# Kernel tuning notes

Hardware: AMD Instinct MI355X
Metric: run time of the kernel (lower is better)

## Reference

```python
import jax, jax.numpy as jnp
import numpy as np

NB_CLASSES = 10
EPS = 1e-8  # torch cosine_similarity eps


def gcn_conv(x, W, b, src, dst, n):
    h = x @ W
    deg = jax.ops.segment_sum(jnp.ones_like(src, dtype=h.dtype), dst, num_segments=n) + 1.0
    dinv = deg ** -0.5
    coef = (dinv[src] * dinv[dst])[:, None]
    agg = jax.ops.segment_sum(h[src] * coef, dst, num_segments=n)
    return agg + h * (1.0 / deg)[:, None] + b


def condition_net(e, w_in, b_in, w_hid, b_hid, w_out, b_out):
    # ConditionNet with num_layers=2: input_fc -> elu -> hidden_fc[0] -> elu -> output_fc
    h = jax.nn.elu(e @ w_in + b_in)
    h = jax.nn.elu(h @ w_hid + b_hid)
    return h @ w_out + b_out


def setup_inputs() -> dict:
    key = jax.random.key(0)
    N, E, D, H, T, M = 20000, 320000, 256, 256, 3, 2048
    ks = jax.random.split(key, 24)
    s = 1.0 / np.sqrt(D)
    inp = {
        "x": jax.random.normal(ks[0], (N, D), dtype=jnp.float32),
        "src": jax.random.randint(ks[1], (E,), 0, N, dtype=jnp.int32),
        "dst": jax.random.randint(ks[2], (E,), 0, N, dtype=jnp.int32),
        "idx": jax.random.randint(ks[3], (M,), 0, N, dtype=jnp.int32),
        "labels": jax.random.randint(ks[4], (M,), 0, NB_CLASSES, dtype=jnp.int32),
        "train": 1,
        # 3 GCNConv layers (all D->D, residual structure forces equal widths)
        "gcn_W1": jax.random.normal(ks[5], (D, D), dtype=jnp.float32) * s,
        "gcn_b1": jnp.zeros((D,), dtype=jnp.float32),
        "gcn_W2": jax.random.normal(ks[6], (D, D), dtype=jnp.float32) * s,
        "gcn_b2": jnp.zeros((D,), dtype=jnp.float32),
        "gcn_W3": jax.random.normal(ks[7], (D, D), dtype=jnp.float32) * s,
        "gcn_b3": jnp.zeros((D,), dtype=jnp.float32),
        # T=3 ConditionNets, params stacked on leading axis
        "cn_w_in": jax.random.normal(ks[8], (T, D, H), dtype=jnp.float32) * s,
        "cn_b_in": jnp.zeros((T, H), dtype=jnp.float32),
        "cn_w_hid": jax.random.normal(ks[9], (T, H, H), dtype=jnp.float32) * s,
        "cn_b_hid": jnp.zeros((T, H), dtype=jnp.float32),
        "cn_w_out": jax.random.normal(ks[10], (T, H, D), dtype=jnp.float32) * s,
        "cn_b_out": jnp.zeros((T, D), dtype=jnp.float32),
        # Embed_prompt
        "p_list": jax.random.normal(ks[11], (5, D), dtype=jnp.float32) * s,
        "a_W": jax.random.normal(ks[12], (D, 5), dtype=jnp.float32) * s,
        "a_b": jnp.zeros((5,), dtype=jnp.float32),
        # gcn_weight2 (trainable); weight1 and weight3 are frozen zeros, closed over
        "gcn_weight2": jnp.float32(1.0),
    }
    return inp


def reference(x, src, dst, idx, labels, train,
              gcn_W1, gcn_b1, gcn_W2, gcn_b2, gcn_W3, gcn_b3,
              cn_w_in, cn_b_in, cn_w_hid, cn_b_hid, cn_w_out, cn_b_out,
              p_list, a_W, a_b, gcn_weight2):
    n = x.shape[0]
    origin_x = x
    w1 = jnp.float32(0.0)  # gcn_weight1 (frozen)
    w3 = jnp.float32(0.0)  # gcn_weight3 (frozen)
    T = cn_w_in.shape[0]
    for t in range(T):  # think layers (small static count)
        e1 = gcn_conv(x, gcn_W1, gcn_b1, src, dst, n)
        e2 = gcn_conv(e1, gcn_W2, gcn_b2, src, dst, n) + e1
        e3 = gcn_conv(e2, gcn_W3, gcn_b3, src, dst, n) + e2
        embed = w1 * e1 + gcn_weight2 * e2 + w3 * e3
        prompt = condition_net(embed, cn_w_in[t], cn_b_in[t], cn_w_hid[t], cn_b_hid[t],
                               cn_w_out[t], cn_b_out[t])
        x = prompt * origin_x
    # full gcn(x, edge_index): 3 convs with ELU activation (standard GCN forward)
    h = jax.nn.elu(gcn_conv(x, gcn_W1, gcn_b1, src, dst, n))
    h = jax.nn.elu(gcn_conv(h, gcn_W2, gcn_b2, src, dst, n))
    h = jax.nn.elu(gcn_conv(h, gcn_W3, gcn_b3, src, dst, n))
    # Embed_prompt: attention over 5 learned prompt vectors
    weight = jax.nn.softmax(h @ a_W + a_b, axis=1)  # [N, 5]
    embed = h + weight @ p_list
    rawret = embed[idx]  # [M, D]
    # train==1: class prototypes via scatter-mean over labels
    sums = jax.ops.segment_sum(rawret, labels, num_segments=NB_CLASSES)
    counts = jax.ops.segment_sum(jnp.ones_like(labels, dtype=rawret.dtype), labels,
                                 num_segments=NB_CLASSES)
    ave = sums / jnp.maximum(counts, 1.0)[:, None]  # [C, D]
    # fused cosine similarity: normalize both, one matmul (replaces M*C scalar loop)
    rn = rawret / jnp.maximum(jnp.linalg.norm(rawret, axis=1, keepdims=True), EPS)
    an = ave / jnp.maximum(jnp.linalg.norm(ave, axis=1, keepdims=True), EPS)
    ret = jax.nn.softmax(rn @ an.T, axis=1)  # [M, C]
    return ret
```

## Files before the change

### kernel.cpp

```cpp
#include <hip/hip_runtime.h>
#include <hip/hip_bf16.h>
#include <math.h>

#define NN 20000
#define DD 256
#define EE 320000
#define MM 2048
#define CC 10
#define TT 3

typedef __attribute__((ext_vector_type(8))) short s8v;
typedef __attribute__((ext_vector_type(4))) float f4v;

__device__ unsigned short g_xb[NN * DD];
__device__ unsigned short g_xo[NN * DD];
__device__ unsigned short g_hb[NN * DD];
__device__ unsigned short g_e1b[NN * DD];
__device__ unsigned short g_e2b[NN * DD];
__device__ int   g_cnt[NN];
__device__ int   g_cursor[NN];
__device__ int   g_rowstart[NN + 1];
__device__ float g_dinv[NN];
__device__ float g_invdeg[NN];
__device__ int   g_part[128];
__device__ int2  g_edge[EE];
__device__ float g_sums[CC * DD];
__device__ float g_cntf[CC];
__device__ unsigned short g_wT1[12 * DD * DD];
__device__ unsigned short g_wT2[12 * DD * DD];

__device__ __forceinline__ float wave_sum(float v) {
#pragma unroll
  for (int off = 32; off > 0; off >>= 1) v += __shfl_xor(v, off);
  return v;
}

__device__ __forceinline__ float eluf(float x) {
  return x > 0.f ? x : expm1f(x);
}

__device__ __forceinline__ float2 bfpair(unsigned int d) {
  union { unsigned int i; float f; } a, b;
  a.i = d << 16;
  b.i = d & 0xffff0000u;
  return make_float2(a.f, b.f);
}

__device__ __forceinline__ unsigned int packbf(float x, float y) {
  union { __hip_bfloat162 v; unsigned int u; } c;
  c.v = __float22bfloat162_rn(make_float2(x, y));
  return c.u;
}

__device__ __forceinline__ void gl_lds16(const unsigned short* g, unsigned short* l) {
  __builtin_amdgcn_global_load_lds(
      (const __attribute__((address_space(1))) unsigned int*)g,
      (__attribute__((address_space(3))) unsigned int*)l, 16, 0, 0);
}

struct WPtrs { const float* p[12]; };

__global__ __launch_bounds__(256) void init_k(const float* __restrict__ x,
                                              unsigned short* __restrict__ xb,
                                              WPtrs wp) {
  __shared__ float t[64][65];
  int b = blockIdx.x;
  int tid = threadIdx.x;
  if (b < 2500) {
    int i = b * 256 + tid;
    const float4* x4 = (const float4*)x;
    float4 a = x4[i * 2], bb = x4[i * 2 + 1];
    uint4 o;
    o.x = packbf(a.x, a.y);
    o.y = packbf(a.z, a.w);
    o.z = packbf(bb.x, bb.y);
    o.w = packbf(bb.z, bb.w);
    ((uint4*)xb)[i] = o;
  } else if (b < 2692) {
    int bb = b - 2500;
    int widx = bb >> 4;
    int rem = bb & 15;
    int kt0 = (rem >> 2) * 64, nt0 = (rem & 3) * 64;
    const float* W = wp.p[widx];
    int ln = tid & 63, lk = tid >> 6;
    for (int kk = lk; kk < 64; kk += 4)
      t[kk][ln] = W[(size_t)(kt0 + kk) * DD + nt0 + ln];
    __syncthreads();
    for (int nn = lk; nn < 64; nn += 4) {
      float v = t[ln][nn];
      __hip_bfloat16 hb = __float2bfloat16(v);
      float hf = __bfloat162float(hb);
      __hip_bfloat16 lb = __float2bfloat16(v - hf);
      union { __hip_bfloat16 b; unsigned short s; } ch, cl;
      ch.b = hb; cl.b = lb;
      size_t o = (size_t)widx * DD * DD + (size_t)(nt0 + nn) * DD + kt0 + ln;
      g_wT1[o] = ch.s;
      g_wT2[o] = cl.s;
    }
  } else {
    int i = (b - 2692) * 256 + tid;
    if (i < NN) { g_cnt[i] = 0; g_cursor[i] = 0; }
    if (i < CC * DD) g_sums[i] = 0.f;
    if (i < CC) g_cntf[i] = 0.f;
  }
}

__global__ void hist_k(const int* __restrict__ dst) {
  int e = blockIdx.x * blockDim.x + threadIdx.x;
  if (e < EE) atomicAdd(&g_cnt[dst[e]], 1);
}

__global__ __launch_bounds__(256) void scanA_k() {
  __shared__ int s[256];
  int t = threadIdx.x;
  int i = blockIdx.x * 256 + t;
  int v = (i < NN) ? g_cnt[i] : 0;
  s[t] = v;
  __syncthreads();
#pragma unroll
  for (int off = 128; off > 0; off >>= 1) {
    if (t < off) s[t] += s[t + off];
    __syncthreads();
  }
  if (t == 0) g_part[blockIdx.x] = s[0];
}

__global__ __launch_bounds__(256) void scanC_k() {
  __shared__ int ps[128];
  __shared__ int s[256];
  int t = threadIdx.x;
  if (t < 128) ps[t] = (t < 79) ? g_part[t] : 0;
  __syncthreads();
#pragma unroll
  for (int off = 1; off < 128; off <<= 1) {
    int v = (t >= off && t < 128) ? ps[t - off] : 0;
    __syncthreads();
    if (t < 128) ps[t] += v;
    __syncthreads();
  }
  int base = (blockIdx.x == 0) ? 0 : ps[blockIdx.x - 1];
  int i = blockIdx.x * 256 + t;
  int v = (i < NN) ? g_cnt[i] : 0;
  s[t] = v;
  __syncthreads();
#pragma unroll
  for (int off = 1; off < 256; off <<= 1) {
    int x2 = (t >= off) ? s[t - off] : 0;
    __syncthreads();
    s[t] += x2;
    __syncthreads();
  }
  if (i < NN) {
    g_rowstart[i] = base + s[t] - v;
    float dg = (float)(v + 1);
    g_invdeg[i] = 1.0f / dg;
    g_dinv[i] = 1.0f / sqrtf(dg);
  }
  if (blockIdx.x == 78 && t == 0) g_rowstart[NN] = EE;
}

__global__ void fill_k(const int* __restrict__ src, const int* __restrict__ dst) {
  int e = blockIdx.x * blockDim.x + threadIdx.x;
  if (e < EE) {
    int d = dst[e];
    int p = atomicAdd(&g_cursor[d], 1);
    int j = g_rowstart[d] + p;
    int si = src[e];
    float coef = g_dinv[si] * g_dinv[d];
    g_edge[j] = make_int2(si * 512, __float_as_int(coef));
  }
}

template <int SPLIT>
union GemmSM {
  unsigned short st[2][(1024 + 512 * SPLIT) * 8];
  float ct[64][68];
};

template <int EPI, int SPLIT>
__global__ __launch_bounds__(256) void gemm_k(const unsigned short* __restrict__ A,
                                              const unsigned short* __restrict__ B1,
                                              const unsigned short* __restrict__ B2,
                                              unsigned short* __restrict__ C,
                                              const float* __restrict__ bias,
                                              const float* __restrict__ alphap,
                                              const unsigned short* __restrict__ mul) {
  __shared__ GemmSM<SPLIT> sm;
  constexpr int CB = 1024 + 512 * SPLIT;
  int b = blockIdx.x;
  int xcd = b & 7, off = b >> 3;
  int logical = (xcd < 4) ? xcd * 157 + off : 628 + (xcd - 4) * 156 + off;
  int mblk = logical >> 2, nblk = logical & 3;
  int row0 = mblk * 64, col0 = nblk * 64;

  int tid = threadIdx.x;
  int wv = tid >> 6, lane = tid & 63;
  int wm = wv >> 1, wn = wv & 1;
  int lr = lane & 15, lk = lane >> 4;

  f4v acc[2][2];
#pragma unroll
  for (int i = 0; i < 2; ++i)
#pragma unroll
    for (int j = 0; j < 2; ++j) acc[i][j] = (f4v){0.f, 0.f, 0.f, 0.f};

  auto stage = [&](int buf, int kt) {
    unsigned short* base = sm.st[buf];
#pragma unroll
    for (int i = 0; i < CB / 256; ++i) {
      int cb = (wv * (CB / 256) + i) * 64;
      int c = cb + lane;
      unsigned short* ldst = base + (size_t)cb * 8;
      if (c < 512) {
        int row = c >> 3, pos = c & 7;
        int kc = pos ^ (row & 7);
        int gr = row0 + row;
        gr = gr < NN ? gr : NN - 1;
        gl_lds16(A + (size_t)gr * DD + kt + kc * 8, ldst);
      } else if (c < 1024) {
        int c2 = c - 512;
        int col = c2 >> 3, pos = c2 & 7;
        int kc = pos ^ (col & 7);
        gl_lds16(B1 + (size_t)(col0 + col) * DD + kt + kc * 8, ldst);
      } else {
        int c2 = c - 1024;
        int col = c2 >> 3, pos = c2 & 7;
        int kc = pos ^ (col & 7);
        gl_lds16(B2 + (size_t)(col0 + col) * DD + kt + kc * 8, ldst);
      }
    }
  };

  stage(0, 0);
  __syncthreads();

  int buf = 0;
#pragma unroll
  for (int t = 0; t < 4; ++t) {
    if (t < 3) stage(buf ^ 1, (t + 1) * 64);
    const unsigned short* base = sm.st[buf];
#pragma unroll
    for (int ksub = 0; ksub < 2; ++ksub) {
      int kc = ksub * 4 + lk;
      s8v a[2], b1v[2], b2v[2];
#pragma unroll
      for (int mi = 0; mi < 2; ++mi) {
        int row = wm * 32 + mi * 16 + lr;
        a[mi] = *(const s8v*)(base + (row * 8 + (kc ^ (row & 7))) * 8);
      }
#pragma unroll
      for (int nj = 0; nj < 2; ++nj) {
        int col = wn * 32 + nj * 16 + lr;
        int ch = col * 8 + (kc ^ (col & 7));
        b1v[nj] = *(const s8v*)(base + (512 + ch) * 8);
        if (SPLIT) b2v[nj] = *(const s8v*)(base + (1024 + ch) * 8);
      }
#pragma unroll
      for (int mi = 0; mi < 2; ++mi)
#pragma unroll
        for (int nj = 0; nj < 2; ++nj) {
          acc[mi][nj] = __builtin_amdgcn_mfma_f32_16x16x32_bf16(a[mi], b1v[nj], acc[mi][nj], 0, 0, 0);
          if (SPLIT)
            acc[mi][nj] = __builtin_amdgcn_mfma_f32_16x16x32_bf16(a[mi], b2v[nj], acc[mi][nj], 0, 0, 0);
        }
    }
    __syncthreads();
    buf ^= 1;
  }

#pragma unroll
  for (int mi = 0; mi < 2; ++mi)
#pragma unroll
    for (int nj = 0; nj < 2; ++nj)
#pragma unroll
      for (int r = 0; r < 4; ++r)
        sm.ct[wm * 32 + mi * 16 + lk * 4 + r][wn * 32 + nj * 16 + lr] = acc[mi][nj][r];
  __syncthreads();

  float alpha = 1.f;
  if (EPI == 1) alpha = alphap ? *alphap : 1.f;
#pragma unroll
  for (int p = 0; p < 2; ++p) {
    int row = p * 32 + (tid >> 3);
    int c0 = (tid & 7) * 8;
    int gr = row0 + row;
    int gc = col0 + c0;
    if (gr < NN) {
      float v[8];
      float4 va = *(float4*)&sm.ct[row][c0];
      float4 vb = *(float4*)&sm.ct[row][c0 + 4];
      v[0] = va.x; v[1] = va.y; v[2] = va.z; v[3] = va.w;
      v[4] = vb.x; v[5] = vb.y; v[6] = vb.z; v[7] = vb.w;
      if (EPI == 1) {
        float4 bv0 = *(const float4*)(bias + gc);
        float4 bv1 = *(const float4*)(bias + gc + 4);
        float bb[8] = {bv0.x, bv0.y, bv0.z, bv0.w, bv1.x, bv1.y, bv1.z, bv1.w};
#pragma unroll
        for (int i = 0; i < 8; ++i) v[i] = eluf(fmaf(alpha, v[i], bb[i]));
      } else if (EPI == 2) {
        float4 bv0 = *(const float4*)(bias + gc);
        float4 bv1 = *(const float4*)(bias + gc + 4);
        float bb[8] = {bv0.x, bv0.y, bv0.z, bv0.w, bv1.x, bv1.y, bv1.z, bv1.w};
        uint4 mu = *(const uint4*)(mul + (size_t)gr * DD + gc);
        float2 m0 = bfpair(mu.x), m1 = bfpair(mu.y), m2 = bfpair(mu.z), m3 = bfpair(mu.w);
        float mm[8] = {m0.x, m0.y, m1.x, m1.y, m2.x, m2.y, m3.x, m3.y};
#pragma unroll
        for (int i = 0; i < 8; ++i) v[i] = (v[i] + bb[i]) * mm[i];
      }
      uint4 o;
      o.x = packbf(v[0], v[1]);
      o.y = packbf(v[2], v[3]);
      o.z = packbf(v[4], v[5]);
      o.w = packbf(v[6], v[7]);
      *(uint4*)(C + (size_t)gr * DD + gc) = o;
    }
  }
}

template <int RES>
__device__ __forceinline__ void agg_row8(int row, int sl, int hf,
                                         const unsigned short* __restrict__ h,
                                         const float* __restrict__ bias,
                                         const unsigned short* __restrict__ res,
                                         float* o) {
  const char* hb = (const char*)h;
  int lo = sl * 16;
  float acc[8];
#pragma unroll
  for (int k = 0; k < 8; ++k) acc[k] = 0.f;
  int s = g_rowstart[row], e = g_rowstart[row + 1];
  int j = s;
  for (; j + 12 <= e; j += 12) {
    int2 E[6];
    uint4 V[6];
#pragma unroll
    for (int u = 0; u < 6; ++u) E[u] = g_edge[j + 2 * u + hf];
#pragma unroll
    for (int u = 0; u < 6; ++u) V[u] = *(const uint4*)(hb + (size_t)E[u].x + lo);
#pragma unroll
    for (int u = 0; u < 6; ++u) {
      float c = __int_as_float(E[u].y);
      float2 p0 = bfpair(V[u].x), p1 = bfpair(V[u].y);
      float2 p2 = bfpair(V[u].z), p3 = bfpair(V[u].w);
      acc[0] = fmaf(c, p0.x, acc[0]); acc[1] = fmaf(c, p0.y, acc[1]);
      acc[2] = fmaf(c, p1.x, acc[2]); acc[3] = fmaf(c, p1.y, acc[3]);
      acc[4] = fmaf(c, p2.x, acc[4]); acc[5] = fmaf(c, p2.y, acc[5]);
      acc[6] = fmaf(c, p3.x, acc[6]); acc[7] = fmaf(c, p3.y, acc[7]);
    }
  }
  for (; j < e; j += 2) {
    int jj = j + hf;
    int jc = jj < e ? jj : e - 1;
    int2 E0 = g_edge[jc];
    uint4 V0 = *(const uint4*)(hb + (size_t)E0.x + lo);
    float c = (jj < e) ? __int_as_float(E0.y) : 0.f;
    float2 p0 = bfpair(V0.x), p1 = bfpair(V0.y);
    float2 p2 = bfpair(V0.z), p3 = bfpair(V0.w);
    acc[0] = fmaf(c, p0.x, acc[0]); acc[1] = fmaf(c, p0.y, acc[1]);
    acc[2] = fmaf(c, p1.x, acc[2]); acc[3] = fmaf(c, p1.y, acc[3]);
    acc[4] = fmaf(c, p2.x, acc[4]); acc[5] = fmaf(c, p2.y, acc[5]);
    acc[6] = fmaf(c, p3.x, acc[6]); acc[7] = fmaf(c, p3.y, acc[7]);
  }
#pragma unroll
  for (int k = 0; k < 8; ++k) acc[k] += __shfl_xor(acc[k], 32);
  float idg = g_invdeg[row];
  uint4 hv = *(const uint4*)(hb + (size_t)row * 512 + lo);
  float2 h0 = bfpair(hv.x), h1 = bfpair(hv.y), h2 = bfpair(hv.z), h3 = bfpair(hv.w);
  float hw[8] = {h0.x, h0.y, h1.x, h1.y, h2.x, h2.y, h3.x, h3.y};
  float4 b0 = *(const float4*)(bias + sl * 8);
  float4 b1 = *(const float4*)(bias + sl * 8 + 4);
  float bb[8] = {b0.x, b0.y, b0.z, b0.w, b1.x, b1.y, b1.z, b1.w};
#pragma unroll
  for (int k = 0; k < 8; ++k) o[k] = acc[k] + hw[k] * idg + bb[k];
  if (RES) {
    uint4 rv = *(const uint4*)((const char*)res + (size_t)row * 512 + lo);
    float2 r0 = bfpair(rv.x), r1 = bfpair(rv.y), r2 = bfpair(rv.z), r3 = bfpair(rv.w);
    float rw[8] = {r0.x, r0.y, r1.x, r1.y, r2.x, r2.y, r3.x, r3.y};
#pragma unroll
    for (int k = 0; k < 8; ++k) o[k] += rw[k];
  }
}

template <int ELU, int RES>
__global__ __launch_bounds__(256) void agg_k(const unsigned short* __restrict__ h,
                                             const float* __restrict__ bias,
                                             const unsigned short* __restrict__ res,
                                             unsigned short* __restrict__ out) {
  int row = (blockIdx.x * 256 + threadIdx.x) >> 6;
  int lane = threadIdx.x & 63;
  int sl = lane & 31, hf = lane >> 5;
  float o[8];
  agg_row8<RES>(row, sl, hf, h, bias, res, o);
  if (ELU) {
#pragma unroll
    for (int k = 0; k < 8; ++k) o[k] = eluf(o[k]);
  }
  if (hf == 0) {
    uint4 pk;
    pk.x = packbf(o[0], o[1]);
    pk.y = packbf(o[2], o[3]);
    pk.z = packbf(o[4], o[5]);
    pk.w = packbf(o[6], o[7]);
    *(uint4*)((char*)out + (size_t)row * 512 + sl * 16) = pk;
  }
}

__device__ __forceinline__ float4 attn_apply(float4 r, int lane,
                                             const float* __restrict__ aW,
                                             const float* __restrict__ ab,
                                             const float* __restrict__ plist) {
  int d = lane * 4;
  float lg[5];
#pragma unroll
  for (int k = 0; k < 5; ++k) {
    float p = r.x * aW[(d + 0) * 5 + k] + r.y * aW[(d + 1) * 5 + k] +
              r.z * aW[(d + 2) * 5 + k] + r.w * aW[(d + 3) * 5 + k];
    lg[k] = wave_sum(p) + ab[k];
  }
  float mx = lg[0];
#pragma unroll
  for (int k = 1; k < 5; ++k) mx = fmaxf(mx, lg[k]);
  float w[5], sum = 0.f;
#pragma unroll
  for (int k = 0; k < 5; ++k) { w[k] = expf(lg[k] - mx); sum += w[k]; }
  float inv = 1.f / sum;
#pragma unroll
  for (int k = 0; k < 5; ++k) {
    float wk = w[k] * inv;
    float4 pv = *(const float4*)(plist + k * DD + d);
    r.x = fmaf(wk, pv.x, r.x);
    r.y = fmaf(wk, pv.y, r.y);
    r.z = fmaf(wk, pv.z, r.z);
    r.w = fmaf(wk, pv.w, r.w);
  }
  return r;
}

__global__ __launch_bounds__(256) void proto_k(const unsigned short* __restrict__ h,
                                               const int* __restrict__ idxp,
                                               const int* __restrict__ labels,
                                               const float* __restrict__ aW,
                                               const float* __restrict__ ab,
                                               const float* __restrict__ plist) {
  __shared__ float sums[CC][DD];
  __shared__ float cnts[CC];
  int t = threadIdx.x;
#pragma unroll
  for (int c = 0; c < CC; ++c) sums[c][t] = 0.f;
  if (t < CC) cnts[t] = 0.f;
  __syncthreads();
  int wv = t >> 6, lane = t & 63;
  int m0 = blockIdx.x * 64 + wv * 16;
  int d = lane * 4;
  for (int rr = 0; rr < 16; ++rr) {
    int m = m0 + rr;
    int row = idxp[m];
    int lab = labels[m];
    uint2 rv = *(const uint2*)((const char*)h + (size_t)row * 512 + lane * 8);
    float2 a0 = bfpair(rv.x), a1 = bfpair(rv.y);
    float4 r = attn_apply(make_float4(a0.x, a0.y, a1.x, a1.y), lane, aW, ab, plist);
    atomicAdd(&sums[lab][d + 0], r.x);
    atomicAdd(&sums[lab][d + 1], r.y);
    atomicAdd(&sums[lab][d + 2], r.z);
    atomicAdd(&sums[lab][d + 3], r.w);
    if (lane == 0) atomicAdd(&cnts[lab], 1.f);
  }
  __syncthreads();
#pragma unroll
  for (int c = 0; c < CC; ++c) atomicAdd(&g_sums[c * DD + t], sums[c][t]);
  if (t < CC) atomicAdd(&g_cntf[t], cnts[t]);
}

__global__ __launch_bounds__(256) void cos_k(const unsigned short* __restrict__ h,
                                             const int* __restrict__ idxp,
                                             const float* __restrict__ aW,
                                             const float* __restrict__ ab,
                                             const float* __restrict__ plist,
                                             float* __restrict__ out) {
  __shared__ float an[CC][DD];
  __shared__ float red[4];
  int t = threadIdx.x;
  int lane = t & 63, wv = t >> 6;
  for (int c = 0; c < CC; ++c) {
    float v = g_sums[c * DD + t] / fmaxf(g_cntf[c], 1.0f);
    float sq = wave_sum(v * v);
    if (lane == 0) red[wv] = sq;
    __syncthreads();
    float tot = red[0] + red[1] + red[2] + red[3];
    float nrm = fmaxf(sqrtf(tot), 1e-8f);
    an[c][t] = v / nrm;
    __syncthreads();
  }
  int wid = (blockIdx.x * 256 + t) >> 6;
  if (wid >= MM) return;
  int row = idxp[wid];
  uint2 rv = *(const uint2*)((const char*)h + (size_t)row * 512 + lane * 8);
  float2 r0 = bfpair(rv.x), r1 = bfpair(rv.y);
  float4 r = attn_apply(make_float4(r0.x, r0.y, r1.x, r1.y), lane, aW, ab, plist);
  float n = wave_sum(r.x * r.x + r.y * r.y + r.z * r.z + r.w * r.w);
  float rnf = 1.0f / fmaxf(sqrtf(n), 1e-8f);
  float lg[CC];
#pragma unroll
  for (int c = 0; c < CC; ++c) {
    float4 a = ((const float4*)&an[c][0])[lane];
    float p = r.x * a.x + r.y * a.y + r.z * a.z + r.w * a.w;
    lg[c] = wave_sum(p) * rnf;
  }
  float mx = lg[0];
#pragma unroll
  for (int c = 1; c < CC; ++c) mx = fmaxf(mx, lg[c]);
  float s = 0.f, w[CC];
#pragma unroll
  for (int c = 0; c < CC; ++c) { w[c] = expf(lg[c] - mx); s += w[c]; }
  float inv = 1.f / s;
#pragma unroll
  for (int c = 0; c < CC; ++c)
    if (lane == c) out[(size_t)wid * CC + c] = w[c] * inv;
}

extern "C" void kernel_launch(void* const* d_in, const int* in_sizes, int n_in,
                              void* d_out, int out_size, void* d_ws, size_t ws_size,
                              hipStream_t stream) {
  (void)in_sizes; (void)n_in; (void)d_ws; (void)ws_size; (void)out_size;
  const float* x      = (const float*)d_in[0];
  const int*   src    = (const int*)d_in[1];
  const int*   dst    = (const int*)d_in[2];
  const int*   idx    = (const int*)d_in[3];
  const int*   labels = (const int*)d_in[4];
  const float* W1 = (const float*)d_in[6];
  const float* b1 = (const float*)d_in[7];
  const float* W2 = (const float*)d_in[8];
  const float* b2 = (const float*)d_in[9];
  const float* W3 = (const float*)d_in[10];
  const float* b3 = (const float*)d_in[11];
  const float* cw_in  = (const float*)d_in[12];
  const float* cb_in  = (const float*)d_in[13];
  const float* cw_hid = (const float*)d_in[14];
  const float* cb_hid = (const float*)d_in[15];
  const float* cw_out = (const float*)d_in[16];
  const float* cb_out = (const float*)d_in[17];
  const float* plist  = (const float*)d_in[18];
  const float* aW     = (const float*)d_in[19];
  const float* ab     = (const float*)d_in[20];
  const float* w2s    = (const float*)d_in[21];
  float* out = (float*)d_out;

  unsigned short *xb, *xo, *hb, *e1b, *e2b, *wt1, *wt2;
  hipGetSymbolAddress((void**)&xb,  HIP_SYMBOL(g_xb));
  hipGetSymbolAddress((void**)&xo,  HIP_SYMBOL(g_xo));
  hipGetSymbolAddress((void**)&hb,  HIP_SYMBOL(g_hb));
  hipGetSymbolAddress((void**)&e1b, HIP_SYMBOL(g_e1b));
  hipGetSymbolAddress((void**)&e2b, HIP_SYMBOL(g_e2b));
  hipGetSymbolAddress((void**)&wt1, HIP_SYMBOL(g_wT1));
  hipGetSymbolAddress((void**)&wt2, HIP_SYMBOL(g_wT2));

  auto WT1 = [&](int w) { return (const unsigned short*)(wt1 + (size_t)w * DD * DD); };
  auto WT2 = [&](int w) { return (const unsigned short*)(wt2 + (size_t)w * DD * DD); };

  WPtrs wp;
  wp.p[0] = W1; wp.p[1] = W2; wp.p[2] = W3;
  for (int t = 0; t < 3; ++t) {
    wp.p[3 + t] = cw_in  + (size_t)t * DD * DD;
    wp.p[6 + t] = cw_hid + (size_t)t * DD * DD;
    wp.p[9 + t] = cw_out + (size_t)t * DD * DD;
  }
  init_k<<<2771, 256, 0, stream>>>(x, xb, wp);
  hist_k<<<1250, 256, 0, stream>>>(dst);
  scanA_k<<<79, 256, 0, stream>>>();
  scanC_k<<<79, 256, 0, stream>>>();
  fill_k<<<1250, 256, 0, stream>>>(src, dst);

  const int GG = 1252;
  const unsigned short* xin = xb;
  for (int t = 0; t < TT; ++t) {
    gemm_k<0, 1><<<GG, 256, 0, stream>>>(xin, WT1(0), WT2(0), hb, nullptr, nullptr, nullptr);
    agg_k<0, 0><<<5000, 256, 0, stream>>>(hb, b1, nullptr, e1b);
    gemm_k<0, 1><<<GG, 256, 0, stream>>>(e1b, WT1(1), WT2(1), hb, nullptr, nullptr, nullptr);
    agg_k<0, 1><<<5000, 256, 0, stream>>>(hb, b2, e1b, e2b);
    gemm_k<1, 0><<<GG, 256, 0, stream>>>(e2b, WT1(3 + t), WT1(3 + t), e1b,
                                         cb_in + (size_t)t * DD, w2s, nullptr);
    gemm_k<1, 0><<<GG, 256, 0, stream>>>(e1b, WT1(6 + t), WT1(6 + t), hb,
                                         cb_hid + (size_t)t * DD, nullptr, nullptr);
    gemm_k<2, 0><<<GG, 256, 0, stream>>>(hb, WT1(9 + t), WT1(9 + t), xo,
                                         cb_out + (size_t)t * DD, nullptr, xb);
    xin = xo;
  }

  gemm_k<0, 1><<<GG, 256, 0, stream>>>(xin, WT1(0), WT2(0), hb, nullptr, nullptr, nullptr);
  agg_k<1, 0><<<5000, 256, 0, stream>>>(hb, b1, nullptr, e1b);
  gemm_k<0, 1><<<GG, 256, 0, stream>>>(e1b, WT1(1), WT2(1), hb, nullptr, nullptr, nullptr);
  agg_k<1, 0><<<5000, 256, 0, stream>>>(hb, b2, nullptr, e2b);
  gemm_k<0, 1><<<GG, 256, 0, stream>>>(e2b, WT1(2), WT2(2), hb, nullptr, nullptr, nullptr);
  agg_k<1, 0><<<5000, 256, 0, stream>>>(hb, b3, nullptr, e1b);

  proto_k<<<32, 256, 0, stream>>>(e1b, idx, labels, aW, ab, plist);
  cos_k<<<512, 256, 0, stream>>>(e1b, idx, aW, ab, plist, out);
}
```

Measured before the change: 556.8 us.

## Aggregate final GCN layer only at indexed rows and batch the edge-loop tail

```diff
diff --git a/kernel.cpp b/kernel.cpp
--- a/kernel.cpp
+++ b/kernel.cpp
@@ -348,18 +348,28 @@
       acc[6] = fmaf(c, p3.x, acc[6]); acc[7] = fmaf(c, p3.y, acc[7]);
     }
   }
-  for (; j < e; j += 2) {
-    int jj = j + hf;
-    int jc = jj < e ? jj : e - 1;
-    int2 E0 = g_edge[jc];
-    uint4 V0 = *(const uint4*)(hb + (size_t)E0.x + lo);
-    float c = (jj < e) ? __int_as_float(E0.y) : 0.f;
-    float2 p0 = bfpair(V0.x), p1 = bfpair(V0.y);
-    float2 p2 = bfpair(V0.z), p3 = bfpair(V0.w);
-    acc[0] = fmaf(c, p0.x, acc[0]); acc[1] = fmaf(c, p0.y, acc[1]);
-    acc[2] = fmaf(c, p1.x, acc[2]); acc[3] = fmaf(c, p1.y, acc[3]);
-    acc[4] = fmaf(c, p2.x, acc[4]); acc[5] = fmaf(c, p2.y, acc[5]);
-    acc[6] = fmaf(c, p3.x, acc[6]); acc[7] = fmaf(c, p3.y, acc[7]);
+  if (j < e) {
+    int2 E[6];
+    uint4 V[6];
+    int live[6];
+#pragma unroll
+    for (int u = 0; u < 6; ++u) {
+      int jj = j + 2 * u + hf;
+      live[u] = jj < e;
+      E[u] = g_edge[live[u] ? jj : e - 1];
+    }
+#pragma unroll
+    for (int u = 0; u < 6; ++u) V[u] = *(const uint4*)(hb + (size_t)E[u].x + lo);
+#pragma unroll
+    for (int u = 0; u < 6; ++u) {
+      float c = live[u] ? __int_as_float(E[u].y) : 0.f;
+      float2 p0 = bfpair(V[u].x), p1 = bfpair(V[u].y);
+      float2 p2 = bfpair(V[u].z), p3 = bfpair(V[u].w);
+      acc[0] = fmaf(c, p0.x, acc[0]); acc[1] = fmaf(c, p0.y, acc[1]);
+      acc[2] = fmaf(c, p1.x, acc[2]); acc[3] = fmaf(c, p1.y, acc[3]);
+      acc[4] = fmaf(c, p2.x, acc[4]); acc[5] = fmaf(c, p2.y, acc[5]);
+      acc[6] = fmaf(c, p3.x, acc[6]); acc[7] = fmaf(c, p3.y, acc[7]);
+    }
   }
 #pragma unroll
   for (int k = 0; k < 8; ++k) acc[k] += __shfl_xor(acc[k], 32);
@@ -405,6 +415,28 @@
   }
 }
 
+__global__ __launch_bounds__(256) void agg_idx_k(const unsigned short* __restrict__ h,
+                                                 const float* __restrict__ bias,
+                                                 const int* __restrict__ idxp,
+                                                 unsigned short* __restrict__ gath) {
+  int m = (blockIdx.x * 256 + threadIdx.x) >> 6;
+  int lane = threadIdx.x & 63;
+  int sl = lane & 31, hf = lane >> 5;
+  int row = idxp[m];
+  float o[8];
+  agg_row8<0>(row, sl, hf, h, bias, nullptr, o);
+#pragma unroll
+  for (int k = 0; k < 8; ++k) o[k] = eluf(o[k]);
+  if (hf == 0) {
+    uint4 pk;
+    pk.x = packbf(o[0], o[1]);
+    pk.y = packbf(o[2], o[3]);
+    pk.z = packbf(o[4], o[5]);
+    pk.w = packbf(o[6], o[7]);
+    *(uint4*)((char*)gath + (size_t)m * 512 + sl * 16) = pk;
+  }
+}
+
 __device__ __forceinline__ float4 attn_apply(float4 r, int lane,
                                              const float* __restrict__ aW,
                                              const float* __restrict__ ab,
@@ -436,8 +468,7 @@
   return r;
 }
 
-__global__ __launch_bounds__(256) void proto_k(const unsigned short* __restrict__ h,
-                                               const int* __restrict__ idxp,
+__global__ __launch_bounds__(256) void proto_k(const unsigned short* __restrict__ gath,
                                                const int* __restrict__ labels,
                                                const float* __restrict__ aW,
                                                const float* __restrict__ ab,
@@ -454,9 +485,8 @@
   int d = lane * 4;
   for (int rr = 0; rr < 16; ++rr) {
     int m = m0 + rr;
-    int row = idxp[m];
     int lab = labels[m];
-    uint2 rv = *(const uint2*)((const char*)h + (size_t)row * 512 + lane * 8);
+    uint2 rv = *(const uint2*)((const char*)gath + (size_t)m * 512 + lane * 8);
     float2 a0 = bfpair(rv.x), a1 = bfpair(rv.y);
     float4 r = attn_apply(make_float4(a0.x, a0.y, a1.x, a1.y), lane, aW, ab, plist);
     atomicAdd(&sums[lab][d + 0], r.x);
@@ -471,8 +501,7 @@
   if (t < CC) atomicAdd(&g_cntf[t], cnts[t]);
 }
 
-__global__ __launch_bounds__(256) void cos_k(const unsigned short* __restrict__ h,
-                                             const int* __restrict__ idxp,
+__global__ __launch_bounds__(256) void cos_k(const unsigned short* __restrict__ gath,
                                              const float* __restrict__ aW,
                                              const float* __restrict__ ab,
                                              const float* __restrict__ plist,
@@ -493,8 +522,7 @@
   }
   int wid = (blockIdx.x * 256 + t) >> 6;
   if (wid >= MM) return;
-  int row = idxp[wid];
-  uint2 rv = *(const uint2*)((const char*)h + (size_t)row * 512 + lane * 8);
+  uint2 rv = *(const uint2*)((const char*)gath + (size_t)wid * 512 + lane * 8);
   float2 r0 = bfpair(rv.x), r1 = bfpair(rv.y);
   float4 r = attn_apply(make_float4(r0.x, r0.y, r1.x, r1.y), lane, aW, ab, plist);
   float n = wave_sum(r.x * r.x + r.y * r.y + r.z * r.z + r.w * r.w);
@@ -591,8 +619,8 @@
   gemm_k<0, 1><<<GG, 256, 0, stream>>>(e1b, WT1(1), WT2(1), hb, nullptr, nullptr, nullptr);
   agg_k<1, 0><<<5000, 256, 0, stream>>>(hb, b2, nullptr, e2b);
   gemm_k<0, 1><<<GG, 256, 0, stream>>>(e2b, WT1(2), WT2(2), hb, nullptr, nullptr, nullptr);
-  agg_k<1, 0><<<5000, 256, 0, stream>>>(hb, b3, nullptr, e1b);
-
-  proto_k<<<32, 256, 0, stream>>>(e1b, idx, labels, aW, ab, plist);
-  cos_k<<<512, 256, 0, stream>>>(e1b, idx, aW, ab, plist, out);
-}
+  agg_idx_k<<<512, 256, 0, stream>>>(hb, b3, idx, e1b);
+
+  proto_k<<<32, 256, 0, stream>>>(e1b, labels, aW, ab, plist);
+  cos_k<<<512, 256, 0, stream>>>(e1b, aW, ab, plist, out);
+}
```

After: 556.5 us. No clear change (-0.1%).
